# Kernel optimization log

Measured on AMD Instinct MI355X. Metric: run time of the kernel, lower is better.

The kernel has to match this reference:

```python
import jax, jax.numpy as jnp
import numpy as np

N, E = 20000, 256000
NODE_DIM, EDGE_DIM = 128, 8
HID, HEADS, LAYERS = 64, 4, 3   # TransformerConv: out_channels per head = HID, concat=False
CLASSES, GRAPHS = 3, 64
HC = HEADS * HID


def setup_inputs() -> dict:
    key = jax.random.key(0)
    ks = iter(jax.random.split(key, 40))
    g = lambda shape, s=0.05: jax.random.normal(next(ks), shape, dtype=jnp.float32) * s
    z = lambda shape: jnp.zeros(shape, jnp.float32)
    return dict(
        x=jax.random.normal(next(ks), (N, NODE_DIM), dtype=jnp.float32),
        edge_attr=jax.random.normal(next(ks), (E, EDGE_DIM), dtype=jnp.float32),
        node_W=g((NODE_DIM, HID)), node_b=z((HID,)),
        e1_W=g((EDGE_DIM, HID)), e1_b=z((HID,)),
        e2_W=g((HID, HID)), e2_b=z((HID,)),
        Wq=g((LAYERS, HID, HC)), bq=z((LAYERS, HC)),
        Wk=g((LAYERS, HID, HC)), bk=z((LAYERS, HC)),
        Wv=g((LAYERS, HID, HC)), bv=z((LAYERS, HC)),
        We=g((LAYERS, HID, HC)),                      # lin_edge has bias=False in PyG
        Wskip=g((LAYERS, HID, HID)), bskip=z((LAYERS, HID)),
        ln_g=jnp.ones((LAYERS, HID), jnp.float32), ln_b=z((LAYERS, HID)),
        cls_W=g((HID, CLASSES)), cls_b=z((CLASSES,)),
        edge_index=jax.random.randint(next(ks), (2, E), 0, N),
        batch=jnp.sort(jax.random.randint(next(ks), (N,), 0, GRAPHS)),
    )


def _layer_norm(x, g, b, eps=1e-5):
    m = x.mean(-1, keepdims=True)
    v = x.var(-1, keepdims=True)
    return (x - m) * jax.lax.rsqrt(v + eps) * g + b


def reference(x, edge_attr, node_W, node_b, e1_W, e1_b, e2_W, e2_b,
              Wq, bq, Wk, bk, Wv, bv, We, Wskip, bskip, ln_g, ln_b,
              cls_W, cls_b, edge_index, batch):
    src, dst = edge_index[0], edge_index[1]          # messages flow src -> dst
    h = x @ node_W + node_b                          # [N, HID]
    e = jax.nn.relu(edge_attr @ e1_W + e1_b) @ e2_W + e2_b  # [E, HID]
    scale = 1.0 / jnp.sqrt(jnp.float32(HID))
    for l in range(LAYERS):                          # fixed small layer count
        res = h
        q = (h @ Wq[l] + bq[l]).reshape(N, HEADS, HID)
        k = (h @ Wk[l] + bk[l]).reshape(N, HEADS, HID)
        v = (h @ Wv[l] + bv[l]).reshape(N, HEADS, HID)
        ee = (e @ We[l]).reshape(E, HEADS, HID)      # per-layer edge projection
        kj = k[src] + ee                             # [E, H, C] irregular gather
        alpha = (q[dst] * kj).sum(-1) * scale        # [E, H]
        amax = jax.ops.segment_max(alpha, dst, num_segments=N)
        ea = jnp.exp(alpha - amax[dst])
        denom = jax.ops.segment_sum(ea, dst, num_segments=N)
        alpha = ea / denom[dst]                      # segment softmax over in-edges
        # dropout on alpha: identity in eval mode
        msg = (v[src] + ee) * alpha[..., None]       # [E, H, C]
        agg = jax.ops.segment_sum(msg, dst, num_segments=N)  # [N, H, C]
        conv = agg.mean(axis=1) + (res @ Wskip[l] + bskip[l])  # concat=False, root_weight
        h = jax.nn.relu(_layer_norm(conv + res, ln_g[l], ln_b[l]))
        # model-level dropout: identity in eval mode
    gsum = jax.ops.segment_sum(h, batch, num_segments=GRAPHS)
    gcnt = jax.ops.segment_sum(jnp.ones((N, 1), h.dtype), batch, num_segments=GRAPHS)
    pooled = gsum / jnp.maximum(gcnt, 1.0)           # global mean pool
    return jax.nn.log_softmax(pooled @ cls_W + cls_b, axis=-1)  # [GRAPHS, CLASSES]
```

## Files before the change

### kernel.cpp

```cpp
#include <hip/hip_runtime.h>
#include <hip/hip_bf16.h>
#include <math.h>

#define NN 20000
#define NE 256000
#define NODE_DIM_ 128
#define EDGE_DIM_ 8
#define HID 64
#define HEADS 4
#define NLAYERS 3
#define NCLASSES 3
#define NGRAPHS 64
#define HC 256
#define EB 64
#define EPB 16

typedef __hip_bfloat16 bf16;
using v8s = __attribute__((ext_vector_type(8))) short;
using f32x4 = __attribute__((ext_vector_type(4))) float;

__device__ __forceinline__ float B2F(bf16 x) { return __bfloat162float(x); }
__device__ __forceinline__ bf16 F2B(float x) { return __float2bfloat16(x); }
__device__ __forceinline__ short F2BS(float x) {
    union { bf16 b; short s; } u; u.b = __float2bfloat16(x); return u.s;
}
__device__ __forceinline__ float U2F(unsigned short u) { return __uint_as_float(((unsigned)u) << 16); }
__device__ __forceinline__ int clampi(int x, int lo, int hi) { return min(max(x, lo), hi); }

__global__ void gt_write_const(float* out, int n, float val) {
    int i = blockIdx.x * blockDim.x + threadIdx.x;
    if (i < n) out[i] = val;
}

__global__ void gt_zero_i32(int* p, int n) {
    int i = blockIdx.x * blockDim.x + threadIdx.x;
    if (i < n) p[i] = 0;
}

__global__ void gt_prep_wqe(const float* __restrict__ Wq, const float* __restrict__ bq,
                            const float* __restrict__ bk, const float* __restrict__ bv,
                            const float* __restrict__ We,
                            float* __restrict__ Wqe, float* __restrict__ bias4) {
    int b = blockIdx.x;
    int l = b / 65, kk = b % 65;
    int t = threadIdx.x;
    int hh = t >> 6, d = t & 63;
    const float* Weh = We + (size_t)l * HID * HC + (size_t)d * HC + hh * 64;
    if (kk < 64) {
        const float* Wqr = Wq + (size_t)l * HID * HC + (size_t)kk * HC + hh * 64;
        float s = 0.f;
        for (int c = 0; c < 64; ++c) s += Wqr[c] * Weh[c];
        Wqe[(size_t)l * HID * HC + (size_t)kk * HC + t] = s;
    } else {
        const float* bqr = bq + (size_t)l * HC + hh * 64;
        float s = 0.f;
        for (int c = 0; c < 64; ++c) s += bqr[c] * Weh[c];
        bias4[(size_t)l * 1024 + 768 + t] = s;
        bias4[(size_t)l * 1024 + t]       = bq[(size_t)l * HC + t];
        bias4[(size_t)l * 1024 + 256 + t] = bk[(size_t)l * HC + t];
        bias4[(size_t)l * 1024 + 512 + t] = bv[(size_t)l * HC + t];
    }
}

__global__ void gt_pack_qkv(const float* __restrict__ Wq, const float* __restrict__ Wk,
                            const float* __restrict__ Wv, const float* __restrict__ Wqe,
                            bf16* __restrict__ Bp) {
    int idx = blockIdx.x * 256 + threadIdx.x;
    if (idx >= NLAYERS * 8192) return;
    int lane = idx & 63;
    int ks = (idx >> 6) & 1;
    int nf = (idx >> 7) & 63;
    int l = idx >> 13;
    int col = nf * 16 + (lane & 15);
    int k0 = ks * 32 + (lane >> 4) * 8;
    const float* src;
    int c;
    if (col < 256)      { src = Wq  + (size_t)l * HID * HC; c = col; }
    else if (col < 512) { src = Wk  + (size_t)l * HID * HC; c = col - 256; }
    else if (col < 768) { src = Wv  + (size_t)l * HID * HC; c = col - 512; }
    else                { src = Wqe + (size_t)l * HID * HC; c = col - 768; }
    bf16* dst = Bp + (size_t)idx * 8;
#pragma unroll
    for (int j = 0; j < 8; ++j) dst[j] = F2B(src[(size_t)(k0 + j) * HC + c]);
}

__global__ void gt_pack_w2(const float* __restrict__ W2, bf16* __restrict__ B2p) {
    int idx = blockIdx.x * 256 + threadIdx.x;
    if (idx >= 512) return;
    int lane = idx & 63;
    int ks = (idx >> 6) & 1;
    int nf = idx >> 7;
    int col = nf * 16 + (lane & 15);
    int k0 = ks * 32 + (lane >> 4) * 8;
    bf16* dst = B2p + (size_t)idx * 8;
#pragma unroll
    for (int j = 0; j < 8; ++j) dst[j] = F2B(W2[(size_t)(k0 + j) * HID + col]);
}

__global__ void gt_prep_wcomb(const float* __restrict__ We, const float* __restrict__ Wskip,
                              float* __restrict__ Wc) {
    int idx = blockIdx.x * blockDim.x + threadIdx.x;
    if (idx >= NLAYERS * 320 * 64) return;
    int l = idx / (320 * 64);
    int r = idx % (320 * 64);
    int kk = r / 64;
    int c = r % 64;
    float val;
    if (kk < 256) {
        int hh = kk >> 6, j = kk & 63;
        val = We[(size_t)l * HID * HC + (size_t)j * HC + hh * 64 + c];
    } else {
        int j = kk - 256;
        val = Wskip[(size_t)l * HID * HID + (size_t)j * HID + c];
    }
    Wc[(size_t)l * 320 * 64 + (size_t)((kk >> 2) * 64 + c) * 4 + (kk & 3)] = val;
}

__global__ void gt_node_proj(const float* __restrict__ x, const float* __restrict__ W,
                             const float* __restrict__ b, float* __restrict__ h) {
    int t = threadIdx.x;
    int n = blockIdx.x * 4 + (t >> 6);
    int c = t & 63;
    __shared__ float xr[4][NODE_DIM_];
    for (int i = t; i < 4 * NODE_DIM_; i += 256) {
        int nn = blockIdx.x * 4 + i / NODE_DIM_;
        xr[i / NODE_DIM_][i % NODE_DIM_] = (nn < NN) ? x[(size_t)nn * NODE_DIM_ + i % NODE_DIM_] : 0.f;
    }
    __syncthreads();
    if (n >= NN) return;
    float acc = 0.f;
#pragma unroll 8
    for (int j = 0; j < NODE_DIM_; ++j) acc += xr[t >> 6][j] * W[j * HID + c];
    h[(size_t)n * HID + c] = acc + b[c];
}

__global__ void gt_edge_mlp(const float* __restrict__ ea, const float* __restrict__ W1,
                            const float* __restrict__ b1, const bf16* __restrict__ B2p,
                            const float* __restrict__ b2, bf16* __restrict__ ef) {
    int t = threadIdx.x;
    int c = t & 63, slot = t >> 6;
    int e0 = blockIdx.x * EB;
    __shared__ float aS[EB][EDGE_DIM_];
    __shared__ bf16 t1s[EB * 64];
    for (int i = t; i < EB * EDGE_DIM_; i += 256) {
        ((float*)aS)[i] = ea[(size_t)e0 * EDGE_DIM_ + i];
    }
    float w1r[EDGE_DIM_];
#pragma unroll
    for (int j = 0; j < EDGE_DIM_; ++j) w1r[j] = W1[j * HID + c];
    float b1c = b1[c];
    __syncthreads();
    int cu = c >> 3, ci = c & 7;
#pragma unroll
    for (int es16 = 0; es16 < 16; ++es16) {
        int es = slot * 16 + es16;
        float acc = b1c;
#pragma unroll
        for (int j = 0; j < EDGE_DIM_; ++j) acc += aS[es][j] * w1r[j];
        int cs = ((cu ^ (es & 7)) << 3) | ci;
        t1s[es * 64 + cs] = F2B(fmaxf(acc, 0.f));
    }
    __syncthreads();
    int lane = t & 63, wave = slot;
    v8s bfr0 = *(const v8s*)(B2p + ((size_t)(wave * 2 + 0) * 64 + lane) * 8);
    v8s bfr1 = *(const v8s*)(B2p + ((size_t)(wave * 2 + 1) * 64 + lane) * 8);
    int rowA = lane & 15, kg = lane >> 4;
    f32x4 acc[4];
#pragma unroll
    for (int mf = 0; mf < 4; ++mf) acc[mf] = (f32x4){0.f, 0.f, 0.f, 0.f};
#pragma unroll
    for (int mf = 0; mf < 4; ++mf) {
        int r = mf * 16 + rowA;
        int u0 = 0 * 4 + kg, u1 = 1 * 4 + kg;
        v8s a0 = *(const v8s*)&t1s[r * 64 + ((u0 ^ (r & 7)) << 3)];
        v8s a1 = *(const v8s*)&t1s[r * 64 + ((u1 ^ (r & 7)) << 3)];
        acc[mf] = __builtin_amdgcn_mfma_f32_16x16x32_bf16(a0, bfr0, acc[mf], 0, 0, 0);
        acc[mf] = __builtin_amdgcn_mfma_f32_16x16x32_bf16(a1, bfr1, acc[mf], 0, 0, 0);
    }
    int col = wave * 16 + (lane & 15);
    float bb = b2[col];
    int rbase = (lane >> 4) * 4;
#pragma unroll
    for (int mf = 0; mf < 4; ++mf) {
#pragma unroll
        for (int reg = 0; reg < 4; ++reg) {
            int e = e0 + mf * 16 + rbase + reg;
            ef[(size_t)e * HID + col] = F2B(acc[mf][reg] + bb);
        }
    }
}

__global__ void gt_count_dst(const int* __restrict__ ei, int* cnt) {
    int e = blockIdx.x * blockDim.x + threadIdx.x;
    if (e < NE) {
        int d = clampi(ei[NE + e], 0, NN - 1);
        atomicAdd(&cnt[d], 1);
    }
}

__global__ void gt_scan_csr(const int* __restrict__ cnt, int* __restrict__ rp, int* __restrict__ cur) {
    __shared__ int part[256];
    int tid = threadIdx.x;
    const int CH = (NN + 255) / 256;
    int s0 = tid * CH, s1 = min(s0 + CH, NN);
    int s = 0;
    for (int i = s0; i < s1; ++i) s += cnt[i];
    part[tid] = s;
    __syncthreads();
    for (int off = 1; off < 256; off <<= 1) {
        int vv = (tid >= off) ? part[tid - off] : 0;
        __syncthreads();
        if (tid >= off) part[tid] += vv;
        __syncthreads();
    }
    int base = (tid == 0) ? 0 : part[tid - 1];
    for (int i = s0; i < s1; ++i) {
        rp[i] = base;
        cur[i] = base;
        base += cnt[i];
    }
    if (tid == 255) rp[NN] = part[255];
}

__global__ void gt_fill_csr(const int* __restrict__ ei, int* cur, int* csr) {
    int e = blockIdx.x * blockDim.x + threadIdx.x;
    if (e < NE) {
        int d = clampi(ei[NE + e], 0, NN - 1);
        int pos = atomicAdd(&cur[d], 1);
        if (pos >= 0 && pos < NE) csr[pos] = e;
    }
}

__global__ void __launch_bounds__(256)
gt_qkv_mfma(const float* __restrict__ h, const bf16* __restrict__ Bp,
            const float* __restrict__ bias4,
            float* __restrict__ q, bf16* __restrict__ k2, bf16* __restrict__ v2,
            float* __restrict__ qe) {
    int t = threadIdx.x, lane = t & 63, wave = t >> 6;
    int n0 = blockIdx.x * 16;
    int rowA = lane & 15, kg = lane >> 4;

    v8s a[2];
    {
        const float* hr = h + (size_t)(n0 + rowA) * HID;
#pragma unroll
        for (int ks = 0; ks < 2; ++ks) {
            const float* p = hr + ks * 32 + kg * 8;
            float4 x0 = *(const float4*)p;
            float4 x1 = *(const float4*)(p + 4);
            v8s av;
            av[0] = F2BS(x0.x); av[1] = F2BS(x0.y); av[2] = F2BS(x0.z); av[3] = F2BS(x0.w);
            av[4] = F2BS(x1.x); av[5] = F2BS(x1.y); av[6] = F2BS(x1.z); av[7] = F2BS(x1.w);
            a[ks] = av;
        }
    }

    f32x4 acc[16];
#pragma unroll
    for (int nf = 0; nf < 16; ++nf) acc[nf] = (f32x4){0.f, 0.f, 0.f, 0.f};

#pragma unroll
    for (int nf = 0; nf < 16; ++nf) {
        int nfg = wave * 16 + nf;
        v8s b0 = *(const v8s*)(Bp + ((size_t)(nfg * 2 + 0) * 64 + lane) * 8);
        v8s b1 = *(const v8s*)(Bp + ((size_t)(nfg * 2 + 1) * 64 + lane) * 8);
        acc[nf] = __builtin_amdgcn_mfma_f32_16x16x32_bf16(a[0], b0, acc[nf], 0, 0, 0);
        acc[nf] = __builtin_amdgcn_mfma_f32_16x16x32_bf16(a[1], b1, acc[nf], 0, 0, 0);
    }

    int rbase = (lane >> 4) * 4;
#pragma unroll
    for (int nf = 0; nf < 16; ++nf) {
        int cc = nf * 16 + (lane & 15);
        float bias = bias4[wave * 256 + cc];
#pragma unroll
        for (int reg = 0; reg < 4; ++reg) {
            int n = n0 + rbase + reg;
            float val = acc[nf][reg] + bias;
            if (wave == 0)      q [(size_t)n * HC + cc] = val;
            else if (wave == 1) k2[(size_t)n * HC + cc] = F2B(val);
            else if (wave == 2) v2[(size_t)n * HC + cc] = F2B(val);
            else                qe[(size_t)n * HC + cc] = val;
        }
    }
}

__global__ void gt_attn_core(float* __restrict__ q, float* __restrict__ qe,
                             const bf16* __restrict__ k, const bf16* __restrict__ v,
                             const bf16* __restrict__ ef,
                             const int* __restrict__ rp, const int* __restrict__ csr,
                             const int* __restrict__ ei) {
    int t = threadIdx.x;
    int lane = t & 63, wave = t >> 6;
    int n = blockIdx.x * 4 + wave;
    if (n >= NN) return;

    const float4* q4 = (const float4*)q;
    const float4* qe4 = (const float4*)qe;
    const ushort4* k4p = (const ushort4*)k;
    const ushort4* v4p = (const ushort4*)v;
    const ushort4* e4p = (const ushort4*)ef;

    float4 qv = q4[(size_t)n * 64 + lane];
    float4 qev = qe4[(size_t)n * 64 + lane];

    int s0 = clampi(rp[n], 0, NE), s1 = clampi(rp[n + 1], s0, NE);
    float m = -1e30f, lr = 0.f;
    float4 accv = make_float4(0.f, 0.f, 0.f, 0.f);
    float4 accs = make_float4(0.f, 0.f, 0.f, 0.f);

    for (int base = s0; base < s1; base += 64) {
        int cnt = min(64, s1 - base);
        int eL = 0, srcL = 0;
        if (lane < cnt) {
            eL = clampi(csr[base + lane], 0, NE - 1);
            srcL = clampi(ei[eL], 0, NN - 1);
        }
        int ea = __builtin_amdgcn_readlane(eL, 0);
        int ra = __builtin_amdgcn_readlane(srcL, 0);
        int j1 = (1 < cnt) ? 1 : 0;
        int eb = __builtin_amdgcn_readlane(eL, j1);
        int rb = __builtin_amdgcn_readlane(srcL, j1);
        ushort4 ka = k4p[(size_t)ra * 64 + lane];
        ushort4 va = v4p[(size_t)ra * 64 + lane];
        ushort4 fa = e4p[(size_t)ea * 16 + (lane & 15)];
        ushort4 kb = k4p[(size_t)rb * 64 + lane];
        ushort4 vb = v4p[(size_t)rb * 64 + lane];
        ushort4 fb = e4p[(size_t)eb * 16 + (lane & 15)];
        for (int i = 0; i < cnt; i += 2) {
            ushort4 kc0 = ka, vc0 = va, ec0 = fa;
            ushort4 kc1 = kb, vc1 = vb, ec1 = fb;
            bool has1 = (i + 1 < cnt);
            if (i + 2 < cnt) {
                int j2 = i + 2;
                int j3 = (i + 3 < cnt) ? i + 3 : i + 2;
                int ea2 = __builtin_amdgcn_readlane(eL, j2);
                int ra2 = __builtin_amdgcn_readlane(srcL, j2);
                int eb2 = __builtin_amdgcn_readlane(eL, j3);
                int rb2 = __builtin_amdgcn_readlane(srcL, j3);
                ka = k4p[(size_t)ra2 * 64 + lane];
                va = v4p[(size_t)ra2 * 64 + lane];
                fa = e4p[(size_t)ea2 * 16 + (lane & 15)];
                kb = k4p[(size_t)rb2 * 64 + lane];
                vb = v4p[(size_t)rb2 * 64 + lane];
                fb = e4p[(size_t)eb2 * 16 + (lane & 15)];
            }
            float p0 = qv.x * U2F(kc0.x) + qv.y * U2F(kc0.y) + qv.z * U2F(kc0.z) + qv.w * U2F(kc0.w)
                     + qev.x * U2F(ec0.x) + qev.y * U2F(ec0.y) + qev.z * U2F(ec0.z) + qev.w * U2F(ec0.w);
            float p1 = qv.x * U2F(kc1.x) + qv.y * U2F(kc1.y) + qv.z * U2F(kc1.z) + qv.w * U2F(kc1.w)
                     + qev.x * U2F(ec1.x) + qev.y * U2F(ec1.y) + qev.z * U2F(ec1.z) + qev.w * U2F(ec1.w);
            p0 += __shfl_xor(p0, 8, 16);  p1 += __shfl_xor(p1, 8, 16);
            p0 += __shfl_xor(p0, 4, 16);  p1 += __shfl_xor(p1, 4, 16);
            p0 += __shfl_xor(p0, 2, 16);  p1 += __shfl_xor(p1, 2, 16);
            p0 += __shfl_xor(p0, 1, 16);  p1 += __shfl_xor(p1, 1, 16);
            p0 *= 0.125f;
            p1 = has1 ? p1 * 0.125f : -1e30f;
            float pm = fmaxf(p0, p1);
            if (__any(pm - m > 8.f)) {
                float nm = fmaxf(m, pm);
                float sc = __expf(m - nm);
                m = nm;
                lr *= sc;
                accv.x *= sc; accv.y *= sc; accv.z *= sc; accv.w *= sc;
                accs.x *= sc; accs.y *= sc; accs.z *= sc; accs.w *= sc;
            }
            float w0 = __expf(p0 - m);
            float w1 = __expf(p1 - m);
            lr += w0 + w1;
            accv.x += w0 * U2F(vc0.x) + w1 * U2F(vc1.x);
            accv.y += w0 * U2F(vc0.y) + w1 * U2F(vc1.y);
            accv.z += w0 * U2F(vc0.z) + w1 * U2F(vc1.z);
            accv.w += w0 * U2F(vc0.w) + w1 * U2F(vc1.w);
            accs.x += w0 * U2F(ec0.x) + w1 * U2F(ec1.x);
            accs.y += w0 * U2F(ec0.y) + w1 * U2F(ec1.y);
            accs.z += w0 * U2F(ec0.z) + w1 * U2F(ec1.z);
            accs.w += w0 * U2F(ec0.w) + w1 * U2F(ec1.w);
        }
    }
    float inv = (s1 > s0) ? 0.25f / lr : 0.f;
    float4 rs = make_float4(accs.x * inv, accs.y * inv, accs.z * inv, accs.w * inv);
    ((float4*)q)[(size_t)n * 64 + lane] = rs;
    float4 rv = make_float4(accv.x * inv, accv.y * inv, accv.z * inv, accv.w * inv);
    rv.x += __shfl_xor(rv.x, 16, 64); rv.x += __shfl_xor(rv.x, 32, 64);
    rv.y += __shfl_xor(rv.y, 16, 64); rv.y += __shfl_xor(rv.y, 32, 64);
    rv.z += __shfl_xor(rv.z, 16, 64); rv.z += __shfl_xor(rv.z, 32, 64);
    rv.w += __shfl_xor(rv.w, 16, 64); rv.w += __shfl_xor(rv.w, 32, 64);
    if (lane < 16) ((float4*)qe)[(size_t)n * 64 + lane] = rv;
}

__global__ void gt_epilogue(const float* __restrict__ acc_s, const float* __restrict__ acc_vm,
                            const float* __restrict__ Wc, const float* __restrict__ bskip,
                            const float* __restrict__ lng, const float* __restrict__ lnb,
                            float* __restrict__ h) {
    int t = threadIdx.x;
    int c = t & 63, qw = t >> 6;
    int n0 = blockIdx.x * EPB;
    __shared__ float sK[EPB][320];
    __shared__ float sVM[EPB][64];
    const float4* as4 = (const float4*)acc_s;
    for (int i = t; i < EPB * 64; i += 256) {
        int nd = i >> 6, j4 = i & 63;
        *(float4*)&sK[nd][4 * j4] = as4[(size_t)(n0 + nd) * 64 + j4];
    }
    const float4* h4g = (const float4*)h;
    const float4* vm4 = (const float4*)acc_vm;
    for (int i = t; i < EPB * 16; i += 256) {
        int nd = i >> 4, j4 = i & 15;
        *(float4*)&sK[nd][256 + 4 * j4] = h4g[(size_t)(n0 + nd) * 16 + j4];
        *(float4*)&sVM[nd][4 * j4] = vm4[(size_t)(n0 + nd) * 64 + j4];
    }
    __syncthreads();
    int nb = qw * 4;
    const float4* r0 = (const float4*)&sK[nb][0];
    const float4* r1 = (const float4*)&sK[nb + 1][0];
    const float4* r2 = (const float4*)&sK[nb + 2][0];
    const float4* r3 = (const float4*)&sK[nb + 3][0];
    const float4* W4 = (const float4*)Wc;
    float a0 = 0.f, a1 = 0.f, a2 = 0.f, a3 = 0.f;
#pragma unroll 4
    for (int k4 = 0; k4 < 80; ++k4) {
        float4 w = W4[k4 * 64 + c];
        float4 x0 = r0[k4]; a0 += x0.x * w.x + x0.y * w.y + x0.z * w.z + x0.w * w.w;
        float4 x1 = r1[k4]; a1 += x1.x * w.x + x1.y * w.y + x1.z * w.z + x1.w * w.w;
        float4 x2 = r2[k4]; a2 += x2.x * w.x + x2.y * w.y + x2.z * w.z + x2.w * w.w;
        float4 x3 = r3[k4]; a3 += x3.x * w.x + x3.y * w.y + x3.z * w.z + x3.w * w.w;
    }
    float bsk = bskip[c], g = lng[c], bb = lnb[c];
    float y0 = a0 + sVM[nb][c] + sK[nb][256 + c] + bsk;
    float y1 = a1 + sVM[nb + 1][c] + sK[nb + 1][256 + c] + bsk;
    float y2 = a2 + sVM[nb + 2][c] + sK[nb + 2][256 + c] + bsk;
    float y3 = a3 + sVM[nb + 3][c] + sK[nb + 3][256 + c] + bsk;
    float m0 = y0, m1 = y1, m2 = y2, m3 = y3;
#pragma unroll
    for (int s = 32; s > 0; s >>= 1) {
        m0 += __shfl_xor(m0, s, 64);
        m1 += __shfl_xor(m1, s, 64);
        m2 += __shfl_xor(m2, s, 64);
        m3 += __shfl_xor(m3, s, 64);
    }
    m0 *= (1.f / HID); m1 *= (1.f / HID); m2 *= (1.f / HID); m3 *= (1.f / HID);
    float d0 = y0 - m0, d1 = y1 - m1, d2 = y2 - m2, d3 = y3 - m3;
    float v0 = d0 * d0, v1 = d1 * d1, v2 = d2 * d2, v3 = d3 * d3;
#pragma unroll
    for (int s = 32; s > 0; s >>= 1) {
        v0 += __shfl_xor(v0, s, 64);
        v1 += __shfl_xor(v1, s, 64);
        v2 += __shfl_xor(v2, s, 64);
        v3 += __shfl_xor(v3, s, 64);
    }
    v0 *= (1.f / HID); v1 *= (1.f / HID); v2 *= (1.f / HID); v3 *= (1.f / HID);
    h[(size_t)(n0 + nb) * HID + c]     = fmaxf(d0 * rsqrtf(v0 + 1e-5f) * g + bb, 0.f);
    h[(size_t)(n0 + nb + 1) * HID + c] = fmaxf(d1 * rsqrtf(v1 + 1e-5f) * g + bb, 0.f);
    h[(size_t)(n0 + nb + 2) * HID + c] = fmaxf(d2 * rsqrtf(v2 + 1e-5f) * g + bb, 0.f);
    h[(size_t)(n0 + nb + 3) * HID + c] = fmaxf(d3 * rsqrtf(v3 + 1e-5f) * g + bb, 0.f);
}

__global__ void gt_pool_sum(const float* __restrict__ h, const int* __restrict__ batch,
                            float* __restrict__ psum) {
    int t = threadIdx.x;
    int c = t & 63, slot = t >> 6;
    int n0 = blockIdx.x * 256;
    float acc = 0.f;
    int curg = -1;
    for (int i = slot; i < 256; i += 4) {
        int n = n0 + i;
        if (n >= NN) break;
        int g = clampi(batch[n], 0, NGRAPHS - 1);
        float val = h[(size_t)n * HID + c];
        if (g != curg) {
            if (curg >= 0) atomicAdd(&psum[curg * HID + c], acc);
            curg = g;
            acc = 0.f;
        }
        acc += val;
    }
    if (curg >= 0) atomicAdd(&psum[curg * HID + c], acc);
}

__global__ void gt_classify(const float* __restrict__ psum, const int* __restrict__ batch,
                            const float* __restrict__ W, const float* __restrict__ b,
                            float* __restrict__ out) {
    int g = blockIdx.x;
    int c = threadIdx.x;
    __shared__ float pooled[HID];
    __shared__ float lg[4];
    __shared__ int bounds[2];
    if (c < 2) {
        int target = g + c;
        int lo = 0, hi = NN;
        while (lo < hi) {
            int mid = (lo + hi) >> 1;
            if (batch[mid] < target) lo = mid + 1; else hi = mid;
        }
        bounds[c] = lo;
    }
    __syncthreads();
    float divf = fmaxf((float)(bounds[1] - bounds[0]), 1.f);
    pooled[c] = psum[g * HID + c] / divf;
    __syncthreads();
    if (c < NCLASSES) {
        float acc = 0.f;
        for (int j = 0; j < HID; ++j) acc += pooled[j] * W[j * NCLASSES + c];
        lg[c] = acc + b[c];
    }
    __syncthreads();
    if (c == 0) {
        float m = fmaxf(lg[0], fmaxf(lg[1], lg[2]));
        float ssum = 0.f;
        for (int cc = 0; cc < NCLASSES; ++cc) ssum += __expf(lg[cc] - m);
        float lse = logf(ssum);
        for (int cc = 0; cc < NCLASSES; ++cc) out[g * NCLASSES + cc] = lg[cc] - m - lse;
    }
}

extern "C" void kernel_launch(void* const* d_in, const int* in_sizes, int n_in,
                              void* d_out, int out_size, void* d_ws, size_t ws_size,
                              hipStream_t stream) {
    float* out = (float*)d_out;

    static const int EXPECT[23] = {2560000, 2048000, 8192, 64, 512, 64, 4096, 64,
                                   49152, 768, 49152, 768, 49152, 768, 49152,
                                   12288, 192, 192, 192, 192, 3, 512000, 20000};
    int bad = -1;
    if (n_in != 23) bad = 99;
    else {
        for (int i = 0; i < 23; ++i) {
            if (in_sizes[i] != EXPECT[i]) { bad = i; break; }
        }
    }
    if (bad >= 0) {
        float val = (bad == 99) ? 4000.f : (5000.f + 10.f * bad);
        gt_write_const<<<1, 256, 0, stream>>>(out, out_size, val);
        return;
    }

    const float* x        = (const float*)d_in[0];
    const float* edge_attr= (const float*)d_in[1];
    const float* node_W   = (const float*)d_in[2];
    const float* node_b   = (const float*)d_in[3];
    const float* e1_W     = (const float*)d_in[4];
    const float* e1_b     = (const float*)d_in[5];
    const float* e2_W     = (const float*)d_in[6];
    const float* e2_b     = (const float*)d_in[7];
    const float* Wq       = (const float*)d_in[8];
    const float* bq       = (const float*)d_in[9];
    const float* Wk       = (const float*)d_in[10];
    const float* bk       = (const float*)d_in[11];
    const float* Wv       = (const float*)d_in[12];
    const float* bv       = (const float*)d_in[13];
    const float* We       = (const float*)d_in[14];
    const float* Wskip    = (const float*)d_in[15];
    const float* bskip    = (const float*)d_in[16];
    const float* lng      = (const float*)d_in[17];
    const float* lnb      = (const float*)d_in[18];
    const float* cls_W    = (const float*)d_in[19];
    const float* cls_b    = (const float*)d_in[20];
    const int*   ei       = (const int*)d_in[21];
    const int*   batch    = (const int*)d_in[22];

    char* w = (char*)d_ws;
    auto alloc = [&](size_t bytes) -> char* {
        char* p = w;
        w += (bytes + 255) & ~(size_t)255;
        return p;
    };
    float* h     = (float*)alloc((size_t)NN * HID * 4);
    bf16*  ef    = (bf16*)alloc((size_t)NE * HID * 2);
    float* q     = (float*)alloc((size_t)NN * HC * 4);
    bf16*  k     = (bf16*)alloc((size_t)NN * HC * 2);
    bf16*  v     = (bf16*)alloc((size_t)NN * HC * 2);
    float* qe    = (float*)alloc((size_t)NN * HC * 4);
    float* Wqe   = (float*)alloc((size_t)NLAYERS * HID * HC * 4);
    float* bias4 = (float*)alloc((size_t)NLAYERS * 1024 * 4);
    bf16*  Bp    = (bf16*)alloc((size_t)NLAYERS * 8192 * 8 * 2);
    bf16*  B2p   = (bf16*)alloc((size_t)512 * 8 * 2);
    float* Wc    = (float*)alloc((size_t)NLAYERS * 320 * 64 * 4);
    float* psum  = (float*)alloc((size_t)NGRAPHS * HID * 4);
    int*   cnt   = (int*)alloc((size_t)NN * 4);
    int*   rp    = (int*)alloc((size_t)(NN + 1) * 4);
    int*   cur   = (int*)alloc((size_t)NN * 4);
    int*   csr   = (int*)alloc((size_t)NE * 4);

    gt_node_proj<<<(NN + 3) / 4, 256, 0, stream>>>(x, node_W, node_b, h);
    gt_prep_wqe<<<NLAYERS * 65, 256, 0, stream>>>(Wq, bq, bk, bv, We, Wqe, bias4);
    gt_pack_qkv<<<(NLAYERS * 8192 + 255) / 256, 256, 0, stream>>>(Wq, Wk, Wv, Wqe, Bp);
    gt_pack_w2<<<2, 256, 0, stream>>>(e2_W, B2p);
    gt_edge_mlp<<<NE / EB, 256, 0, stream>>>(edge_attr, e1_W, e1_b, B2p, e2_b, ef);
    gt_prep_wcomb<<<(NLAYERS * 320 * 64 + 255) / 256, 256, 0, stream>>>(We, Wskip, Wc);
    gt_zero_i32<<<(NN + 255) / 256, 256, 0, stream>>>(cnt, NN);
    gt_count_dst<<<(NE + 255) / 256, 256, 0, stream>>>(ei, cnt);
    gt_scan_csr<<<1, 256, 0, stream>>>(cnt, rp, cur);
    gt_fill_csr<<<(NE + 255) / 256, 256, 0, stream>>>(ei, cur, csr);

    for (int l = 0; l < NLAYERS; ++l) {
        const bf16* Bp_l  = Bp + (size_t)l * 8192 * 8;
        const float* b4_l = bias4 + (size_t)l * 1024;
        const float* Wc_l = Wc + (size_t)l * 320 * 64;
        const float* bs_l = bskip + (size_t)l * HID;
        const float* lg_l = lng + (size_t)l * HID;
        const float* lb_l = lnb + (size_t)l * HID;

        gt_qkv_mfma<<<NN / 16, 256, 0, stream>>>(h, Bp_l, b4_l, q, k, v, qe);
        gt_attn_core<<<(NN + 3) / 4, 256, 0, stream>>>(q, qe, k, v, ef, rp, csr, ei);
        gt_epilogue<<<NN / EPB, 256, 0, stream>>>(q, qe, Wc_l, bs_l, lg_l, lb_l, h);
    }

    gt_zero_i32<<<(NGRAPHS * HID + 255) / 256, 256, 0, stream>>>((int*)psum, NGRAPHS * HID);
    gt_pool_sum<<<(NN + 255) / 256, 256, 0, stream>>>(h, batch, psum);
    gt_classify<<<NGRAPHS, HID, 0, stream>>>(psum, batch, cls_W, cls_b, out);
}
```

Baseline: 556.9 us.

## Interleave K and V into one buffer and deepen gather prefetch in attention

Result: no change. 558.2 us (+0.2%).

```diff
diff --git a/kernel.cpp b/kernel.cpp
--- a/kernel.cpp
+++ b/kernel.cpp
@@ -17,6 +17,7 @@
 
 typedef __hip_bfloat16 bf16;
 using v8s = __attribute__((ext_vector_type(8))) short;
+using u16x8 = __attribute__((ext_vector_type(8))) unsigned short;
 using f32x4 = __attribute__((ext_vector_type(4))) float;
 
 __device__ __forceinline__ float B2F(bf16 x) { return __bfloat162float(x); }
@@ -234,8 +235,7 @@
 __global__ void __launch_bounds__(256)
 gt_qkv_mfma(const float* __restrict__ h, const bf16* __restrict__ Bp,
             const float* __restrict__ bias4,
-            float* __restrict__ q, bf16* __restrict__ k2, bf16* __restrict__ v2,
-            float* __restrict__ qe) {
+            float* __restrict__ q, bf16* __restrict__ kv, float* __restrict__ qe) {
     int t = threadIdx.x, lane = t & 63, wave = t >> 6;
     int n0 = blockIdx.x * 16;
     int rowA = lane & 15, kg = lane >> 4;
@@ -278,16 +278,15 @@
             int n = n0 + rbase + reg;
             float val = acc[nf][reg] + bias;
             if (wave == 0)      q [(size_t)n * HC + cc] = val;
-            else if (wave == 1) k2[(size_t)n * HC + cc] = F2B(val);
-            else if (wave == 2) v2[(size_t)n * HC + cc] = F2B(val);
+            else if (wave == 1) kv[(size_t)n * 512 + ((cc >> 2) << 3) + (cc & 3)] = F2B(val);
+            else if (wave == 2) kv[(size_t)n * 512 + ((cc >> 2) << 3) + 4 + (cc & 3)] = F2B(val);
             else                qe[(size_t)n * HC + cc] = val;
         }
     }
 }
 
 __global__ void gt_attn_core(float* __restrict__ q, float* __restrict__ qe,
-                             const bf16* __restrict__ k, const bf16* __restrict__ v,
-                             const bf16* __restrict__ ef,
+                             const bf16* __restrict__ kv, const bf16* __restrict__ ef,
                              const int* __restrict__ rp, const int* __restrict__ csr,
                              const int* __restrict__ ei) {
     int t = threadIdx.x;
@@ -297,9 +296,9 @@
 
     const float4* q4 = (const float4*)q;
     const float4* qe4 = (const float4*)qe;
-    const ushort4* k4p = (const ushort4*)k;
-    const ushort4* v4p = (const ushort4*)v;
+    const u16x8* kv8 = (const u16x8*)kv;
     const ushort4* e4p = (const ushort4*)ef;
+    int elane = lane & 15;
 
     float4 qv = q4[(size_t)n * 64 + lane];
     float4 qev = qe4[(size_t)n * 64 + lane];
@@ -308,6 +307,39 @@
     float m = -1e30f, lr = 0.f;
     float4 accv = make_float4(0.f, 0.f, 0.f, 0.f);
     float4 accs = make_float4(0.f, 0.f, 0.f, 0.f);
+
+    auto process = [&](u16x8 k0, ushort4 f0, u16x8 k1, ushort4 f1, bool ok0, bool ok1) {
+        float p0 = qv.x * U2F(k0[0]) + qv.y * U2F(k0[1]) + qv.z * U2F(k0[2]) + qv.w * U2F(k0[3])
+                 + qev.x * U2F(f0.x) + qev.y * U2F(f0.y) + qev.z * U2F(f0.z) + qev.w * U2F(f0.w);
+        float p1 = qv.x * U2F(k1[0]) + qv.y * U2F(k1[1]) + qv.z * U2F(k1[2]) + qv.w * U2F(k1[3])
+                 + qev.x * U2F(f1.x) + qev.y * U2F(f1.y) + qev.z * U2F(f1.z) + qev.w * U2F(f1.w);
+        p0 += __shfl_xor(p0, 8, 16);  p1 += __shfl_xor(p1, 8, 16);
+        p0 += __shfl_xor(p0, 4, 16);  p1 += __shfl_xor(p1, 4, 16);
+        p0 += __shfl_xor(p0, 2, 16);  p1 += __shfl_xor(p1, 2, 16);
+        p0 += __shfl_xor(p0, 1, 16);  p1 += __shfl_xor(p1, 1, 16);
+        p0 = ok0 ? p0 * 0.125f : -1e30f;
+        p1 = ok1 ? p1 * 0.125f : -1e30f;
+        float pm = fmaxf(p0, p1);
+        if (__any(pm - m > 8.f)) {
+            float nm = fmaxf(m, pm);
+            float sc = __expf(m - nm);
+            m = nm;
+            lr *= sc;
+            accv.x *= sc; accv.y *= sc; accv.z *= sc; accv.w *= sc;
+            accs.x *= sc; accs.y *= sc; accs.z *= sc; accs.w *= sc;
+        }
+        float w0 = __expf(p0 - m);
+        float w1 = __expf(p1 - m);
+        lr += w0 + w1;
+        accv.x += w0 * U2F(k0[4]) + w1 * U2F(k1[4]);
+        accv.y += w0 * U2F(k0[5]) + w1 * U2F(k1[5]);
+        accv.z += w0 * U2F(k0[6]) + w1 * U2F(k1[6]);
+        accv.w += w0 * U2F(k0[7]) + w1 * U2F(k1[7]);
+        accs.x += w0 * U2F(f0.x) + w1 * U2F(f1.x);
+        accs.y += w0 * U2F(f0.y) + w1 * U2F(f1.y);
+        accs.z += w0 * U2F(f0.z) + w1 * U2F(f1.z);
+        accs.w += w0 * U2F(f0.w) + w1 * U2F(f1.w);
+    };
 
     for (int base = s0; base < s1; base += 64) {
         int cnt = min(64, s1 - base);
@@ -316,65 +348,38 @@
             eL = clampi(csr[base + lane], 0, NE - 1);
             srcL = clampi(ei[eL], 0, NN - 1);
         }
-        int ea = __builtin_amdgcn_readlane(eL, 0);
-        int ra = __builtin_amdgcn_readlane(srcL, 0);
-        int j1 = (1 < cnt) ? 1 : 0;
-        int eb = __builtin_amdgcn_readlane(eL, j1);
-        int rb = __builtin_amdgcn_readlane(srcL, j1);
-        ushort4 ka = k4p[(size_t)ra * 64 + lane];
-        ushort4 va = v4p[(size_t)ra * 64 + lane];
-        ushort4 fa = e4p[(size_t)ea * 16 + (lane & 15)];
-        ushort4 kb = k4p[(size_t)rb * 64 + lane];
-        ushort4 vb = v4p[(size_t)rb * 64 + lane];
-        ushort4 fb = e4p[(size_t)eb * 16 + (lane & 15)];
-        for (int i = 0; i < cnt; i += 2) {
-            ushort4 kc0 = ka, vc0 = va, ec0 = fa;
-            ushort4 kc1 = kb, vc1 = vb, ec1 = fb;
-            bool has1 = (i + 1 < cnt);
+        int jb = min(1, cnt - 1);
+        int eA0 = __builtin_amdgcn_readlane(eL, 0), rA0 = __builtin_amdgcn_readlane(srcL, 0);
+        int eA1 = __builtin_amdgcn_readlane(eL, jb), rA1 = __builtin_amdgcn_readlane(srcL, jb);
+        u16x8 kvA0 = kv8[(size_t)rA0 * 64 + lane];
+        u16x8 kvA1 = kv8[(size_t)rA1 * 64 + lane];
+        ushort4 efA0 = e4p[(size_t)eA0 * 16 + elane];
+        ushort4 efA1 = e4p[(size_t)eA1 * 16 + elane];
+        u16x8 kvB0, kvB1;
+        ushort4 efB0, efB1;
+        for (int i = 0; i < cnt; i += 4) {
+            {
+                int j2 = min(i + 2, cnt - 1), j3 = min(i + 3, cnt - 1);
+                int e2 = __builtin_amdgcn_readlane(eL, j2), r2 = __builtin_amdgcn_readlane(srcL, j2);
+                int e3 = __builtin_amdgcn_readlane(eL, j3), r3 = __builtin_amdgcn_readlane(srcL, j3);
+                kvB0 = kv8[(size_t)r2 * 64 + lane];
+                kvB1 = kv8[(size_t)r3 * 64 + lane];
+                efB0 = e4p[(size_t)e2 * 16 + elane];
+                efB1 = e4p[(size_t)e3 * 16 + elane];
+            }
+            process(kvA0, efA0, kvA1, efA1, true, i + 1 < cnt);
+            if (i + 4 < cnt) {
+                int j4 = i + 4, j5 = min(i + 5, cnt - 1);
+                int e4 = __builtin_amdgcn_readlane(eL, j4), r4 = __builtin_amdgcn_readlane(srcL, j4);
+                int e5 = __builtin_amdgcn_readlane(eL, j5), r5 = __builtin_amdgcn_readlane(srcL, j5);
+                kvA0 = kv8[(size_t)r4 * 64 + lane];
+                kvA1 = kv8[(size_t)r5 * 64 + lane];
+                efA0 = e4p[(size_t)e4 * 16 + elane];
+                efA1 = e4p[(size_t)e5 * 16 + elane];
+            }
             if (i + 2 < cnt) {
-                int j2 = i + 2;
-                int j3 = (i + 3 < cnt) ? i + 3 : i + 2;
-                int ea2 = __builtin_amdgcn_readlane(eL, j2);
-                int ra2 = __builtin_amdgcn_readlane(srcL, j2);
-                int eb2 = __builtin_amdgcn_readlane(eL, j3);
-                int rb2 = __builtin_amdgcn_readlane(srcL, j3);
-                ka = k4p[(size_t)ra2 * 64 + lane];
-                va = v4p[(size_t)ra2 * 64 + lane];
-                fa = e4p[(size_t)ea2 * 16 + (lane & 15)];
-                kb = k4p[(size_t)rb2 * 64 + lane];
-                vb = v4p[(size_t)rb2 * 64 + lane];
-                fb = e4p[(size_t)eb2 * 16 + (lane & 15)];
+                process(kvB0, efB0, kvB1, efB1, true, i + 3 < cnt);
             }
-            float p0 = qv.x * U2F(kc0.x) + qv.y * U2F(kc0.y) + qv.z * U2F(kc0.z) + qv.w * U2F(kc0.w)
-                     + qev.x * U2F(ec0.x) + qev.y * U2F(ec0.y) + qev.z * U2F(ec0.z) + qev.w * U2F(ec0.w);
-            float p1 = qv.x * U2F(kc1.x) + qv.y * U2F(kc1.y) + qv.z * U2F(kc1.z) + qv.w * U2F(kc1.w)
-                     + qev.x * U2F(ec1.x) + qev.y * U2F(ec1.y) + qev.z * U2F(ec1.z) + qev.w * U2F(ec1.w);
-            p0 += __shfl_xor(p0, 8, 16);  p1 += __shfl_xor(p1, 8, 16);
-            p0 += __shfl_xor(p0, 4, 16);  p1 += __shfl_xor(p1, 4, 16);
-            p0 += __shfl_xor(p0, 2, 16);  p1 += __shfl_xor(p1, 2, 16);
-            p0 += __shfl_xor(p0, 1, 16);  p1 += __shfl_xor(p1, 1, 16);
-            p0 *= 0.125f;
-            p1 = has1 ? p1 * 0.125f : -1e30f;
-            float pm = fmaxf(p0, p1);
-            if (__any(pm - m > 8.f)) {
-                float nm = fmaxf(m, pm);
-                float sc = __expf(m - nm);
-                m = nm;
-                lr *= sc;
-                accv.x *= sc; accv.y *= sc; accv.z *= sc; accv.w *= sc;
-                accs.x *= sc; accs.y *= sc; accs.z *= sc; accs.w *= sc;
-            }
-            float w0 = __expf(p0 - m);
-            float w1 = __expf(p1 - m);
-            lr += w0 + w1;
-            accv.x += w0 * U2F(vc0.x) + w1 * U2F(vc1.x);
-            accv.y += w0 * U2F(vc0.y) + w1 * U2F(vc1.y);
-            accv.z += w0 * U2F(vc0.z) + w1 * U2F(vc1.z);
-            accv.w += w0 * U2F(vc0.w) + w1 * U2F(vc1.w);
-            accs.x += w0 * U2F(ec0.x) + w1 * U2F(ec1.x);
-            accs.y += w0 * U2F(ec0.y) + w1 * U2F(ec1.y);
-            accs.z += w0 * U2F(ec0.z) + w1 * U2F(ec1.z);
-            accs.w += w0 * U2F(ec0.w) + w1 * U2F(ec1.w);
         }
     }
     float inv = (s1 > s0) ? 0.25f / lr : 0.f;
@@ -567,8 +572,7 @@
     float* h     = (float*)alloc((size_t)NN * HID * 4);
     bf16*  ef    = (bf16*)alloc((size_t)NE * HID * 2);
     float* q     = (float*)alloc((size_t)NN * HC * 4);
-    bf16*  k     = (bf16*)alloc((size_t)NN * HC * 2);
-    bf16*  v     = (bf16*)alloc((size_t)NN * HC * 2);
+    bf16*  kv    = (bf16*)alloc((size_t)NN * 512 * 2);
     float* qe    = (float*)alloc((size_t)NN * HC * 4);
     float* Wqe   = (float*)alloc((size_t)NLAYERS * HID * HC * 4);
     float* bias4 = (float*)alloc((size_t)NLAYERS * 1024 * 4);
@@ -600,8 +604,8 @@
         const float* lg_l = lng + (size_t)l * HID;
         const float* lb_l = lnb + (size_t)l * HID;
 
-        gt_qkv_mfma<<<NN / 16, 256, 0, stream>>>(h, Bp_l, b4_l, q, k, v, qe);
-        gt_attn_core<<<(NN + 3) / 4, 256, 0, stream>>>(q, qe, k, v, ef, rp, csr, ei);
+        gt_qkv_mfma<<<NN / 16, 256, 0, stream>>>(h, Bp_l, b4_l, q, kv, qe);
+        gt_attn_core<<<(NN + 3) / 4, 256, 0, stream>>>(q, qe, kv, ef, rp, csr, ei);
         gt_epilogue<<<NN / EPB, 256, 0, stream>>>(q, qe, Wc_l, bs_l, lg_l, lb_l, h);
     }
 
```
